# Performance work log

Hardware: AMD Instinct MI355X
Metric: run time of the kernel (lower is better)

## Reference

```python
import jax, jax.numpy as jnp
import numpy as np


def setup_inputs() -> dict:
    key = jax.random.key(0)
    B, C, H, W = 16, 3, 512, 512
    num_bins = 8
    # Bin geometry exactly as in HistLayer.__init__
    bin_edges = np.linspace(-0.05, 1.05, num_bins + 1)
    half_width = (bin_edges[2] - bin_edges[1]) / 2.0
    centers = (bin_edges + half_width)[:-1]  # [num_bins]
    return {
        "input_image": jax.random.uniform(key, (B, C, H, W), dtype=jnp.float32),
        "centers": jnp.asarray(centers, dtype=jnp.float32),   # bin_centers_conv bias = -centers
        "width": jnp.float32(half_width),                      # bin_widths_conv bias
    }


def reference(input_image, centers, width):
    """Differentiable hard-binning histogram (fused form of the grouped 1x1 convs).

    bin_centers_conv (weight=1, bias=-c) -> x - c, broadcast over num_bins
    abs
    bin_widths_conv (weight=-1, bias=w) -> w - |x - c|
    1.01 ** z, then Threshold(1, 0): keep values > 1 else 0
    two_d: flatten spatial; one_d: global average pool (normalize=True path).
    """
    B, C, H, W = input_image.shape
    NB = centers.shape[0]
    # [B, C, NB, H, W]: per-channel broadcast against every bin center
    z = width - jnp.abs(input_image[:, :, None, :, :] - centers[None, None, :, None, None])
    p = jnp.power(jnp.asarray(1.01, input_image.dtype), z)
    xx = jnp.where(p > 1, p, jnp.zeros((), input_image.dtype))
    xx = xx.reshape(B, C * NB, H * W)
    two_d = xx
    one_d = xx.mean(axis=2)  # AdaptiveAvgPool2d(1) then flatten
    return one_d, two_d
```

## Files before the change

kernel.cpp:

```cpp
#include <hip/hip_runtime.h>
#include <math.h>

namespace {
constexpr int NBINS = 8;
constexpr int HW4 = (512 * 512) / 4;
constexpr int PLANES = 16 * 3;
constexpr double LN_BASE = 0.0099503214108481;
constexpr double KEEP_THRESH = 1.0 + 1.0 / 16777216.0;
constexpr float LOG2_BASE = 0.014355293f;

typedef float v4f __attribute__((ext_vector_type(4)));

__device__ __forceinline__ float binval(float z) {
  if (!(z > 0.0f)) return 0.0f;
  if (z < 1.0e-5f) {
    double p = exp((double)z * LN_BASE);
    if (!(p > KEEP_THRESH)) return 0.0f;
  }
  return exp2f(z * LOG2_BASE);
}
}

__global__ __launch_bounds__(256) void hist_kernel(
    const float4* __restrict__ in, const float* __restrict__ centers,
    const float* __restrict__ wptr, float* __restrict__ out) {
  const int plane = blockIdx.y;
  const int i4 = blockIdx.x * 256 + threadIdx.x;
  const float w = wptr[0];
  float c[NBINS];
#pragma unroll
  for (int k = 0; k < NBINS; ++k) c[k] = centers[k];

  const float4 x = in[(size_t)plane * HW4 + i4];
  v4f* const out2 = reinterpret_cast<v4f*>(out + PLANES * NBINS) +
                    (size_t)plane * NBINS * HW4 + i4;
  float sums[NBINS];
#pragma unroll
  for (int k = 0; k < NBINS; ++k) {
    v4f v;
    v.x = binval(w - fabsf(x.x - c[k]));
    v.y = binval(w - fabsf(x.y - c[k]));
    v.z = binval(w - fabsf(x.z - c[k]));
    v.w = binval(w - fabsf(x.w - c[k]));
    __builtin_nontemporal_store(v, out2 + (size_t)k * HW4);
    sums[k] = (v.x + v.y) + (v.z + v.w);
  }

#pragma unroll
  for (int k = 0; k < NBINS; ++k) {
#pragma unroll
    for (int off = 32; off > 0; off >>= 1)
      sums[k] += __shfl_down(sums[k], off, 64);
  }
  __shared__ float part[4][NBINS];
  const int lane = threadIdx.x & 63;
  const int wv = threadIdx.x >> 6;
  if (lane == 0) {
#pragma unroll
    for (int k = 0; k < NBINS; ++k) part[wv][k] = sums[k];
  }
  __syncthreads();
  if (threadIdx.x < NBINS) {
    float s = (part[0][threadIdx.x] + part[1][threadIdx.x]) +
              (part[2][threadIdx.x] + part[3][threadIdx.x]);
    atomicAdd(out + plane * NBINS + threadIdx.x, s * (1.0f / 262144.0f));
  }
}

extern "C" void kernel_launch(void* const* d_in, const int* in_sizes, int n_in,
                              void* d_out, int out_size, void* d_ws, size_t ws_size,
                              hipStream_t stream) {
  const float4* in = (const float4*)d_in[0];
  const float* centers = (const float*)d_in[1];
  const float* width = (const float*)d_in[2];
  float* out = (float*)d_out;
  (void)hipMemsetAsync(d_out, 0, PLANES * NBINS * sizeof(float), stream);
  hist_kernel<<<dim3(256, PLANES), 256, 0, stream>>>(in, centers, width, out);
}
```

Before: 430.6 us.

## Compute only max-bin exponential per element and process four vectors per thread

Each thread now handles four float4 inputs instead of one, with the grid cut by four. Since bins do not overlap, at most one bin per element can be positive, so the kernel takes the max z across bins and evaluates the exponential once per element rather than eight times. The nontemporal stores are replaced with plain stores. This relies on bins not overlapping, and a tie in z would write the value to two bins. The kernel is likely write-bandwidth bound, so the gain may be small.

```diff
diff --git a/kernel.cpp b/kernel.cpp
--- a/kernel.cpp
+++ b/kernel.cpp
@@ -3,8 +3,11 @@
 
 namespace {
 constexpr int NBINS = 8;
-constexpr int HW4 = (512 * 512) / 4;
+constexpr int HW = 512 * 512;
+constexpr int HW4 = HW / 4;
 constexpr int PLANES = 16 * 3;
+constexpr int TPB = 256;
+constexpr int IPT = 4;
 constexpr double LN_BASE = 0.0099503214108481;
 constexpr double KEEP_THRESH = 1.0 + 1.0 / 16777216.0;
 constexpr float LOG2_BASE = 0.014355293f;
@@ -21,29 +24,58 @@
 }
 }
 
-__global__ __launch_bounds__(256) void hist_kernel(
+__global__ __launch_bounds__(TPB) void hist_kernel(
     const float4* __restrict__ in, const float* __restrict__ centers,
     const float* __restrict__ wptr, float* __restrict__ out) {
   const int plane = blockIdx.y;
-  const int i4 = blockIdx.x * 256 + threadIdx.x;
+  const int base = blockIdx.x * (TPB * IPT) + threadIdx.x;
   const float w = wptr[0];
   float c[NBINS];
 #pragma unroll
   for (int k = 0; k < NBINS; ++k) c[k] = centers[k];
 
-  const float4 x = in[(size_t)plane * HW4 + i4];
+  float4 x[IPT];
+#pragma unroll
+  for (int g = 0; g < IPT; ++g)
+    x[g] = in[(size_t)plane * HW4 + base + g * TPB];
+
   v4f* const out2 = reinterpret_cast<v4f*>(out + PLANES * NBINS) +
-                    (size_t)plane * NBINS * HW4 + i4;
+                    (size_t)plane * NBINS * HW4;
+
   float sums[NBINS];
 #pragma unroll
-  for (int k = 0; k < NBINS; ++k) {
-    v4f v;
-    v.x = binval(w - fabsf(x.x - c[k]));
-    v.y = binval(w - fabsf(x.y - c[k]));
-    v.z = binval(w - fabsf(x.z - c[k]));
-    v.w = binval(w - fabsf(x.w - c[k]));
-    __builtin_nontemporal_store(v, out2 + (size_t)k * HW4);
-    sums[k] = (v.x + v.y) + (v.z + v.w);
+  for (int k = 0; k < NBINS; ++k) sums[k] = 0.0f;
+
+#pragma unroll
+  for (int g = 0; g < IPT; ++g) {
+    const int i4 = base + g * TPB;
+    const float px[4] = {x[g].x, x[g].y, x[g].z, x[g].w};
+    v4f zb[NBINS];
+    float zmax[4], val[4];
+#pragma unroll
+    for (int e = 0; e < 4; ++e) {
+      float m = w - fabsf(px[e] - c[0]);
+      zb[0][e] = m;
+#pragma unroll
+      for (int k = 1; k < NBINS; ++k) {
+        const float zk = w - fabsf(px[e] - c[k]);
+        zb[k][e] = zk;
+        m = fmaxf(m, zk);
+      }
+      zmax[e] = m;
+      val[e] = binval(m);
+    }
+#pragma unroll
+    for (int k = 0; k < NBINS; ++k) {
+      v4f v;
+#pragma unroll
+      for (int e = 0; e < 4; ++e) {
+        const float o = (zb[k][e] == zmax[e]) ? val[e] : 0.0f;
+        v[e] = o;
+        sums[k] += o;
+      }
+      out2[(size_t)k * HW4 + i4] = v;
+    }
   }
 
 #pragma unroll
@@ -52,7 +84,7 @@
     for (int off = 32; off > 0; off >>= 1)
       sums[k] += __shfl_down(sums[k], off, 64);
   }
-  __shared__ float part[4][NBINS];
+  __shared__ float part[TPB / 64][NBINS];
   const int lane = threadIdx.x & 63;
   const int wv = threadIdx.x >> 6;
   if (lane == 0) {
@@ -63,7 +95,7 @@
   if (threadIdx.x < NBINS) {
     float s = (part[0][threadIdx.x] + part[1][threadIdx.x]) +
               (part[2][threadIdx.x] + part[3][threadIdx.x]);
-    atomicAdd(out + plane * NBINS + threadIdx.x, s * (1.0f / 262144.0f));
+    atomicAdd(out + plane * NBINS + threadIdx.x, s * (1.0f / (float)HW));
   }
 }
 
@@ -75,5 +107,6 @@
   const float* width = (const float*)d_in[2];
   float* out = (float*)d_out;
   (void)hipMemsetAsync(d_out, 0, PLANES * NBINS * sizeof(float), stream);
-  hist_kernel<<<dim3(256, PLANES), 256, 0, stream>>>(in, centers, width, out);
+  hist_kernel<<<dim3(HW4 / (TPB * IPT), PLANES), TPB, 0, stream>>>(
+      in, centers, width, out);
 }
```

Result: slower. 440.1 us (+2.2%).
